# Kernel tuning notes

Hardware: AMD Instinct MI355X
Metric: run time of the kernel (lower is better)

## Reference

```python
import jax, jax.numpy as jnp
import numpy as np

N_NODES = 100000
N_EDGES = 1_600_000


def _glorot(key, shape):
    fan_in, fan_out = shape
    s = jnp.sqrt(6.0 / (fan_in + fan_out)).astype(jnp.float32)
    return jax.random.uniform(key, shape, jnp.float32, -1.0, 1.0) * s


def setup_inputs() -> dict:
    key = jax.random.key(0)
    ks = jax.random.split(key, 6)
    x = jax.random.normal(ks[0], (N_NODES, 88), jnp.float32)
    edge_index = jax.random.randint(ks[1], (2, N_EDGES), 0, N_NODES, dtype=jnp.int32)
    return {
        "x": x,
        "W1": _glorot(ks[2], (88, 65)), "b1": jnp.zeros((65,), jnp.float32),
        "W2": _glorot(ks[3], (65, 50)), "b2": jnp.zeros((50,), jnp.float32),
        "W3": _glorot(ks[4], (50, 65)), "b3": jnp.zeros((65,), jnp.float32),
        "W4": _glorot(ks[5], (65, 88)), "b4": jnp.zeros((88,), jnp.float32),
        "edge_index": edge_index,
    }


def _gcn_conv(h, W, b, src, dst, norm, n):
    # PyG GCNConv: transform, then normalized neighbor aggregation (self-loops
    # already folded into src/dst/norm).
    h = h @ W                                  # [N, out]
    msg = h[src] * norm[:, None]               # [E+N, out] gather
    return jax.ops.segment_sum(msg, dst, num_segments=n) + b  # scatter-add


def reference(x, W1, b1, W2, b2, W3, b3, W4, b4, edge_index):
    n = x.shape[0]
    loop = jnp.arange(n, dtype=edge_index.dtype)
    src = jnp.concatenate([edge_index[0], loop])   # add self-loops
    dst = jnp.concatenate([edge_index[1], loop])
    deg = jax.ops.segment_sum(jnp.ones_like(dst, dtype=x.dtype), dst, num_segments=n)
    dinv = jnp.where(deg > 0, jax.lax.rsqrt(deg), 0.0)
    norm = dinv[src] * dinv[dst]                   # D^-1/2 (A+I) D^-1/2 edge weights

    # encoder
    h = jax.nn.relu(_gcn_conv(x, W1, b1, src, dst, norm, n))
    h = _gcn_conv(h, W2, b2, src, dst, norm, n)
    # decoder
    h = jax.nn.relu(_gcn_conv(h, W3, b3, src, dst, norm, n))
    return _gcn_conv(h, W4, b4, src, dst, norm, n)
```

## Files before the change

kernel.cpp:

```cpp
#include <hip/hip_runtime.h>

#define BS 256
#define FB 1024
#define NB 256
#define CHUNK 4096
#define CAP 64
#define LCAP 8192

using half4 = __attribute__((ext_vector_type(4))) _Float16;

template<typename T>
__device__ __forceinline__ float4 load4(const T* p) {
    if constexpr (sizeof(T) == 4) {
        return *(const float4*)p;
    } else {
        half4 v = *(const half4*)p;
        return make_float4((float)v.x, (float)v.y, (float)v.z, (float)v.w);
    }
}
template<typename T>
__device__ __forceinline__ void store4(T* p, float4 v) {
    if constexpr (sizeof(T) == 4) {
        *(float4*)p = v;
    } else {
        half4 h = {(_Float16)v.x, (_Float16)v.y, (_Float16)v.z, (_Float16)v.w};
        *(half4*)p = h;
    }
}


__global__ __launch_bounds__(BS) void k_zero1(int* a, int n) {
    int i = blockIdx.x * BS + threadIdx.x;
    if (i < n) a[i] = 0;
}

__global__ __launch_bounds__(BS) void k_bucket(const int* __restrict__ src, const int* __restrict__ dst,
                                               unsigned* __restrict__ bbuf, int* __restrict__ bcounts,
                                               int E, unsigned long long invB, int bsz) {
    __shared__ int lcnt[NB];
    for (int t = threadIdx.x; t < NB; t += BS) lcnt[t] = 0;
    __syncthreads();
    int base_e = blockIdx.x * CHUNK;
    unsigned* mybuf = bbuf + (size_t)blockIdx.x * NB * CAP;
    #pragma unroll
    for (int j = 0; j < CHUNK / BS; ++j) {
        int e = base_e + j * BS + threadIdx.x;
        if (e < E) {
            int d = dst[e];
            int s = src[e];
            int b = (int)(((unsigned long long)(unsigned)d * invB) >> 40);
            int doff = d - b * bsz;
            int pos = atomicAdd(&lcnt[b], 1);
            if (pos < CAP)
                mybuf[b * CAP + pos] = ((unsigned)doff << 17) | (unsigned)s;
        }
    }
    __syncthreads();
    for (int t = threadIdx.x; t < NB; t += BS)
        bcounts[blockIdx.x * NB + t] = min(lcnt[t], CAP);
}

__global__ __launch_bounds__(FB) void k_cnt(const unsigned* __restrict__ bbuf, const int* __restrict__ bcounts,
                                            int* __restrict__ cnt, int nch, int bsz, int N) {
    __shared__ int lhist[512];
    for (int t = threadIdx.x; t < 512; t += FB) lhist[t] = 0;
    __syncthreads();
    int b = blockIdx.x;
    int lo = b * bsz;
    int total = nch * CAP;
    for (int idx = threadIdx.x; idx < total; idx += FB) {
        int seg = idx >> 6, slot = idx & 63;
        int c = bcounts[seg * NB + b];
        if (slot < c)
            atomicAdd(&lhist[bbuf[((size_t)seg * NB + b) * CAP + slot] >> 17], 1);
    }
    __syncthreads();
    int hi = min(N, lo + bsz);
    for (int t = threadIdx.x; t < hi - lo; t += FB) cnt[lo + t] = lhist[t];
}

__global__ __launch_bounds__(BS) void k_dinv(const int* __restrict__ cnt, float* __restrict__ dinv, int N) {
    int i = blockIdx.x * BS + threadIdx.x;
    if (i < N) dinv[i] = rsqrtf((float)(cnt[i] + 1));
}

__global__ __launch_bounds__(BS) void k_scan1(const int* __restrict__ cnt, int* __restrict__ bsum, int N) {
    __shared__ int s[BS];
    int i = blockIdx.x * BS + threadIdx.x;
    s[threadIdx.x] = (i < N) ? cnt[i] : 0;
    __syncthreads();
    for (int off = BS / 2; off > 0; off >>= 1) {
        if (threadIdx.x < off) s[threadIdx.x] += s[threadIdx.x + off];
        __syncthreads();
    }
    if (threadIdx.x == 0) bsum[blockIdx.x] = s[0];
}

__global__ __launch_bounds__(512) void k_scan2(int* bsum, int nb) {
    __shared__ int s[512];
    int t = threadIdx.x;
    int v = (t < nb) ? bsum[t] : 0;
    s[t] = v;
    __syncthreads();
    for (int off = 1; off < 512; off <<= 1) {
        int u = (t >= off) ? s[t - off] : 0;
        __syncthreads();
        s[t] += u;
        __syncthreads();
    }
    if (t < nb) bsum[t] = s[t] - v;
}

__global__ __launch_bounds__(BS) void k_scan3(const int* __restrict__ cnt, const int* __restrict__ boff,
                                              int* __restrict__ row_ptr, int N) {
    __shared__ int s[BS];
    int t = threadIdx.x;
    int i = blockIdx.x * BS + t;
    int v = (i < N) ? cnt[i] : 0;
    s[t] = v;
    __syncthreads();
    for (int off = 1; off < BS; off <<= 1) {
        int u = (t >= off) ? s[t - off] : 0;
        __syncthreads();
        s[t] += u;
        __syncthreads();
    }
    int base = boff[blockIdx.x];
    if (i < N) row_ptr[i] = base + s[t] - v;
    if (i == N - 1) row_ptr[N] = base + s[t];
}

__global__ __launch_bounds__(FB) void k_fill2(const unsigned* __restrict__ bbuf, const int* __restrict__ bcounts,
                                              const int* __restrict__ row_ptr, const float* __restrict__ dinv,
                                              uint2* __restrict__ entries,
                                              int nch, int bsz, int N) {
    __shared__ int cur[512];
    __shared__ float ldinv[512];
    __shared__ unsigned sorted[LCAP];

    int b = blockIdx.x;
    int lo = b * bsz;
    int hi = min(N, lo + bsz);
    int gbase = row_ptr[lo];
    int tot = row_ptr[hi] - gbase;
    for (int t = threadIdx.x; t < hi - lo; t += FB) {
        cur[t] = row_ptr[lo + t] - gbase;
        ldinv[t] = dinv[lo + t];
    }
    __syncthreads();

    int total = nch * CAP;
    for (int idx = threadIdx.x; idx < total; idx += FB) {
        int seg = idx >> 6, slot = idx & 63;
        int c = bcounts[seg * NB + b];
        if (slot < c) {
            unsigned u = bbuf[((size_t)seg * NB + b) * CAP + slot];
            int p = atomicAdd(&cur[u >> 17], 1);
            if (p < LCAP) sorted[p] = u;
        }
    }
    __syncthreads();

    for (int t = threadIdx.x; t < tot; t += FB) {
        unsigned u = sorted[t];
        int s = (int)(u & 0x1FFFFu);
        int doff = (int)(u >> 17);
        float w = dinv[s] * ldinv[doff];
        entries[gbase + t] = make_uint2((unsigned)s, __float_as_uint(w));
    }
}

template<typename TIN, int K, int M, int LDIN, int LDOUT, bool BIAS, bool RELU, typename TOUT>
__global__ __launch_bounds__(BS) void k_gemm(const TIN* __restrict__ H, const float* __restrict__ Wg,
                                             const float* __restrict__ bias, TOUT* __restrict__ out, int N) {
    constexpr int M4 = (M + 3) & ~3;
    __shared__ float Wl[K * M4];
    for (int idx = threadIdx.x; idx < K * M4; idx += BS) {
        int k = idx / M4, m = idx - k * M4;
        Wl[idx] = (m < M) ? Wg[(size_t)k * M + m] : 0.f;
    }
    __syncthreads();

    int row = blockIdx.x * BS + threadIdx.x;
    bool ok = row < N;
    int rr = ok ? row : (N - 1);
    const TIN* hp = H + (size_t)rr * LDIN;

    float acc[M4];
    #pragma unroll
    for (int m = 0; m < M4; ++m) acc[m] = 0.f;

    constexpr int K4 = K & ~3;
    #pragma unroll 2
    for (int k = 0; k < K4; k += 4) {
        float4 hv = load4(hp + k);
        const float h[4] = {hv.x, hv.y, hv.z, hv.w};
        #pragma unroll
        for (int j = 0; j < 4; ++j) {
            const float* wl = &Wl[(k + j) * M4];
            #pragma unroll
            for (int m = 0; m < M4; m += 4) {
                float4 w = *(const float4*)(wl + m);
                acc[m + 0] = fmaf(h[j], w.x, acc[m + 0]);
                acc[m + 1] = fmaf(h[j], w.y, acc[m + 1]);
                acc[m + 2] = fmaf(h[j], w.z, acc[m + 2]);
                acc[m + 3] = fmaf(h[j], w.w, acc[m + 3]);
            }
        }
    }
    #pragma unroll
    for (int k = K4; k < K; ++k) {
        float h = (float)hp[k];
        const float* wl = &Wl[k * M4];
        #pragma unroll
        for (int m = 0; m < M4; m += 4) {
            float4 w = *(const float4*)(wl + m);
            acc[m + 0] = fmaf(h, w.x, acc[m + 0]);
            acc[m + 1] = fmaf(h, w.y, acc[m + 1]);
            acc[m + 2] = fmaf(h, w.z, acc[m + 2]);
            acc[m + 3] = fmaf(h, w.w, acc[m + 3]);
        }
    }

    if (!ok) return;
    TOUT* op = out + (size_t)row * LDOUT;
    #pragma unroll
    for (int g = 0; g < LDOUT / 4; ++g) {
        int cb = 4 * g;
        float4 v;
        float* vp = &v.x;
        #pragma unroll
        for (int j = 0; j < 4; ++j) {
            int c = cb + j;
            float x = (c < M) ? acc[(c < M4) ? c : 0] : 0.f;
            if (BIAS && c < M) x += bias[c];
            if (RELU) x = fmaxf(x, 0.f);
            vp[j] = x;
        }
        store4(op + cb, v);
    }
}

template<typename TIN, typename TOUT, int M, int M4, int LDI, int LDO, bool BIAS, bool RELU>
__global__ __launch_bounds__(BS) void k_agg(const TIN* __restrict__ T, TOUT* __restrict__ out,
                                            const int* __restrict__ row_ptr, const uint2* __restrict__ entries,
                                            const float* __restrict__ dinv, const float* __restrict__ bias,
                                            int N) {
    constexpr int CG = M4 / 4;
    int idx = blockIdx.x * BS + threadIdx.x;
    if (idx >= N * CG) return;
    int i  = idx / CG;
    int cg = idx - i * CG;
    int c0 = cg * 4;

    float di = dinv[i];
    float4 t0 = load4(T + (size_t)i * LDI + c0);
    float w0 = di * di;
    float4 acc0 = make_float4(w0 * t0.x, w0 * t0.y, w0 * t0.z, w0 * t0.w);
    float4 acc1 = make_float4(0.f, 0.f, 0.f, 0.f);

    int e0 = row_ptr[i], e1 = row_ptr[i + 1];
    int e = e0;
    for (; e + 3 < e1; e += 4) {
        uint2 ea = entries[e];
        uint2 eb = entries[e + 1];
        uint2 ec = entries[e + 2];
        uint2 ed = entries[e + 3];
        float4 ta = load4(T + (size_t)ea.x * LDI + c0);
        float4 tb = load4(T + (size_t)eb.x * LDI + c0);
        float4 tc = load4(T + (size_t)ec.x * LDI + c0);
        float4 td = load4(T + (size_t)ed.x * LDI + c0);
        float wa = __uint_as_float(ea.y), wb = __uint_as_float(eb.y);
        float wc = __uint_as_float(ec.y), wd = __uint_as_float(ed.y);
        acc0.x = fmaf(wa, ta.x, acc0.x); acc0.y = fmaf(wa, ta.y, acc0.y);
        acc0.z = fmaf(wa, ta.z, acc0.z); acc0.w = fmaf(wa, ta.w, acc0.w);
        acc1.x = fmaf(wb, tb.x, acc1.x); acc1.y = fmaf(wb, tb.y, acc1.y);
        acc1.z = fmaf(wb, tb.z, acc1.z); acc1.w = fmaf(wb, tb.w, acc1.w);
        acc0.x = fmaf(wc, tc.x, acc0.x); acc0.y = fmaf(wc, tc.y, acc0.y);
        acc0.z = fmaf(wc, tc.z, acc0.z); acc0.w = fmaf(wc, tc.w, acc0.w);
        acc1.x = fmaf(wd, td.x, acc1.x); acc1.y = fmaf(wd, td.y, acc1.y);
        acc1.z = fmaf(wd, td.z, acc1.z); acc1.w = fmaf(wd, td.w, acc1.w);
    }
    for (; e < e1; ++e) {
        uint2 ea = entries[e];
        float4 ta = load4(T + (size_t)ea.x * LDI + c0);
        float wa = __uint_as_float(ea.y);
        acc0.x = fmaf(wa, ta.x, acc0.x); acc0.y = fmaf(wa, ta.y, acc0.y);
        acc0.z = fmaf(wa, ta.z, acc0.z); acc0.w = fmaf(wa, ta.w, acc0.w);
    }
    acc0.x += acc1.x; acc0.y += acc1.y; acc0.z += acc1.z; acc0.w += acc1.w;

    float* vp = &acc0.x;
    #pragma unroll
    for (int j = 0; j < 4; ++j) {
        if (BIAS && (c0 + j) < M) vp[j] += bias[c0 + j];
        if (RELU) vp[j] = fmaxf(vp[j], 0.f);
    }
    store4(out + (size_t)i * LDO + c0, acc0);
}


extern "C" void kernel_launch(void* const* d_in, const int* in_sizes, int n_in,
                              void* d_out, int out_size, void* d_ws, size_t ws_size,
                              hipStream_t stream) {
    const float* x  = (const float*)d_in[0];
    const float* W1 = (const float*)d_in[1];
    const float* b1 = (const float*)d_in[2];
    const float* W2 = (const float*)d_in[3];
    const float* b2 = (const float*)d_in[4];
    const float* W3 = (const float*)d_in[5];
    const float* b3 = (const float*)d_in[6];
    const float* W4 = (const float*)d_in[7];
    const float* b4 = (const float*)d_in[8];
    const int* edge_index = (const int*)d_in[9];

    const int N = in_sizes[0] / 88;
    const int E = in_sizes[9] / 2;
    const int* src = edge_index;
    const int* dst = edge_index + E;

    const int nch = (E + CHUNK - 1) / CHUNK;
    const int bsz = (N + NB - 1) / NB;
    const unsigned long long invB = ((1ull << 40) + bsz - 1) / bsz;

    char* p = (char*)d_ws;
    auto carve = [&](size_t bytes) { void* r = p; p += (bytes + 255) & ~(size_t)255; return r; };
    int*   cnt     = (int*)  carve((size_t)N * 4);
    float* dinv    = (float*)carve((size_t)N * 4);
    int*   row_ptr = (int*)  carve((size_t)(N + 1) * 4);
    int*   bsum    = (int*)  carve(4096);
    int*   bcounts = (int*)  carve((size_t)nch * NB * 4);
    unsigned* bbuf = (unsigned*)carve((size_t)nch * NB * CAP * 4);
    uint2* entries = (uint2*)carve((size_t)E * 8);
    _Float16* hA   = (_Float16*)carve((size_t)N * 68 * 2);
    _Float16* hB   = (_Float16*)carve((size_t)N * 68 * 2);
    _Float16* hC   = (_Float16*)carve((size_t)N * 68 * 2);

    int gN = (N + BS - 1) / BS;

    k_zero1 <<<gN, BS, 0, stream>>>(cnt, N);
    k_bucket<<<nch, BS, 0, stream>>>(src, dst, bbuf, bcounts, E, invB, bsz);
    k_cnt   <<<NB, FB, 0, stream>>>(bbuf, bcounts, cnt, nch, bsz, N);
    k_dinv  <<<gN, BS, 0, stream>>>(cnt, dinv, N);
    k_scan1 <<<gN, BS, 0, stream>>>(cnt, bsum, N);
    k_scan2 <<<1, 512, 0, stream>>>(bsum, gN);
    k_scan3 <<<gN, BS, 0, stream>>>(cnt, bsum, row_ptr, N);
    k_fill2 <<<NB, FB, 0, stream>>>(bbuf, bcounts, row_ptr, dinv, entries, nch, bsz, N);

    auto agg_grid = [&](int CG) { return (N * CG + BS - 1) / BS; };

    k_gemm<float, 88, 65, 88, 68, false, false, _Float16><<<gN, BS, 0, stream>>>(x, W1, nullptr, hA, N);
    k_agg<_Float16, _Float16, 65, 68, 68, 68, true, true><<<agg_grid(17), BS, 0, stream>>>(hA, hB, row_ptr, entries, dinv, b1, N);
    k_gemm<_Float16, 65, 50, 68, 64, false, false, _Float16><<<gN, BS, 0, stream>>>(hB, W2, nullptr, hC, N);
    k_agg<_Float16, _Float16, 50, 52, 64, 64, true, false><<<agg_grid(13), BS, 0, stream>>>(hC, hA, row_ptr, entries, dinv, b2, N);
    k_agg<_Float16, _Float16, 50, 52, 64, 52, false, false><<<agg_grid(13), BS, 0, stream>>>(hA, hB, row_ptr, entries, dinv, nullptr, N);
    k_gemm<_Float16, 50, 65, 52, 68, true, true, _Float16><<<gN, BS, 0, stream>>>(hB, W3, b3, hC, N);
    k_agg<_Float16, _Float16, 65, 68, 68, 68, false, false><<<agg_grid(17), BS, 0, stream>>>(hC, hA, row_ptr, entries, dinv, nullptr, N);
    k_gemm<_Float16, 65, 88, 68, 88, true, false, float><<<gN, BS, 0, stream>>>(hA, W4, b4, (float*)d_out, N);
}
```

Before: 491.7 us.

## Split dense GEMM work so each thread computes two rows by four columns

The node-feature GEMM used to give each thread one full output row, holding every output column in registers. It now gives each thread a 4-column group for two adjacent rows, and the launch grid is sized to match. This spreads the work over many more threads and cuts per-thread register pressure, which should raise occupancy and improve load-balancing. In exchange, each input row is loaded redundantly by several threads (mostly served from cache), and padding columns beyond M4 are no longer zero-filled.

Result: slower. 810.3 us (+64.8%).

```diff
diff --git a/kernel.cpp b/kernel.cpp
--- a/kernel.cpp
+++ b/kernel.cpp
@@ -170,10 +170,16 @@
     }
 }
 
+__device__ __forceinline__ void fma4(float4& a, float s, float4 w) {
+    a.x = fmaf(s, w.x, a.x); a.y = fmaf(s, w.y, a.y);
+    a.z = fmaf(s, w.z, a.z); a.w = fmaf(s, w.w, a.w);
+}
+
 template<typename TIN, int K, int M, int LDIN, int LDOUT, bool BIAS, bool RELU, typename TOUT>
 __global__ __launch_bounds__(BS) void k_gemm(const TIN* __restrict__ H, const float* __restrict__ Wg,
                                              const float* __restrict__ bias, TOUT* __restrict__ out, int N) {
     constexpr int M4 = (M + 3) & ~3;
+    constexpr int CG = M4 / 4;
     __shared__ float Wl[K * M4];
     for (int idx = threadIdx.x; idx < K * M4; idx += BS) {
         int k = idx / M4, m = idx - k * M4;
@@ -181,64 +187,58 @@
     }
     __syncthreads();
 
-    int row = blockIdx.x * BS + threadIdx.x;
-    bool ok = row < N;
-    int rr = ok ? row : (N - 1);
-    const TIN* hp = H + (size_t)rr * LDIN;
-
-    float acc[M4];
-    #pragma unroll
-    for (int m = 0; m < M4; ++m) acc[m] = 0.f;
+    int nrb = (N + 1) >> 1;
+    int idx = blockIdx.x * BS + threadIdx.x;
+    if (idx >= nrb * CG) return;
+    int rb = idx / CG;
+    int cg = idx - rb * CG;
+    int c0 = cg * 4;
+    int r0 = rb * 2;
+    bool two = (r0 + 1 < N);
+    int r1 = two ? r0 + 1 : r0;
+    const TIN* h0 = H + (size_t)r0 * LDIN;
+    const TIN* h1 = H + (size_t)r1 * LDIN;
+
+    float4 a0 = make_float4(0.f, 0.f, 0.f, 0.f);
+    float4 a1 = make_float4(0.f, 0.f, 0.f, 0.f);
 
     constexpr int K4 = K & ~3;
-    #pragma unroll 2
+    #pragma unroll
     for (int k = 0; k < K4; k += 4) {
-        float4 hv = load4(hp + k);
-        const float h[4] = {hv.x, hv.y, hv.z, hv.w};
-        #pragma unroll
-        for (int j = 0; j < 4; ++j) {
-            const float* wl = &Wl[(k + j) * M4];
-            #pragma unroll
-            for (int m = 0; m < M4; m += 4) {
-                float4 w = *(const float4*)(wl + m);
-                acc[m + 0] = fmaf(h[j], w.x, acc[m + 0]);
-                acc[m + 1] = fmaf(h[j], w.y, acc[m + 1]);
-                acc[m + 2] = fmaf(h[j], w.z, acc[m + 2]);
-                acc[m + 3] = fmaf(h[j], w.w, acc[m + 3]);
-            }
-        }
+        float4 p = load4(h0 + k);
+        float4 q = load4(h1 + k);
+        const float* wl = &Wl[k * M4 + c0];
+        float4 w0 = *(const float4*)(wl);
+        float4 w1 = *(const float4*)(wl + M4);
+        float4 w2 = *(const float4*)(wl + 2 * M4);
+        float4 w3 = *(const float4*)(wl + 3 * M4);
+        fma4(a0, p.x, w0); fma4(a1, q.x, w0);
+        fma4(a0, p.y, w1); fma4(a1, q.y, w1);
+        fma4(a0, p.z, w2); fma4(a1, q.z, w2);
+        fma4(a0, p.w, w3); fma4(a1, q.w, w3);
     }
     #pragma unroll
     for (int k = K4; k < K; ++k) {
-        float h = (float)hp[k];
-        const float* wl = &Wl[k * M4];
-        #pragma unroll
-        for (int m = 0; m < M4; m += 4) {
-            float4 w = *(const float4*)(wl + m);
-            acc[m + 0] = fmaf(h, w.x, acc[m + 0]);
-            acc[m + 1] = fmaf(h, w.y, acc[m + 1]);
-            acc[m + 2] = fmaf(h, w.z, acc[m + 2]);
-            acc[m + 3] = fmaf(h, w.w, acc[m + 3]);
-        }
-    }
-
-    if (!ok) return;
-    TOUT* op = out + (size_t)row * LDOUT;
-    #pragma unroll
-    for (int g = 0; g < LDOUT / 4; ++g) {
-        int cb = 4 * g;
-        float4 v;
-        float* vp = &v.x;
-        #pragma unroll
-        for (int j = 0; j < 4; ++j) {
-            int c = cb + j;
-            float x = (c < M) ? acc[(c < M4) ? c : 0] : 0.f;
-            if (BIAS && c < M) x += bias[c];
-            if (RELU) x = fmaxf(x, 0.f);
-            vp[j] = x;
-        }
-        store4(op + cb, v);
-    }
+        float p = (float)h0[k];
+        float q = (float)h1[k];
+        float4 w = *(const float4*)&Wl[k * M4 + c0];
+        fma4(a0, p, w); fma4(a1, q, w);
+    }
+
+    float* p0 = &a0.x;
+    float* p1 = &a1.x;
+    #pragma unroll
+    for (int j = 0; j < 4; ++j) {
+        int c = c0 + j;
+        bool in = (c < M);
+        float bb = (BIAS && in) ? bias[c] : 0.f;
+        float v0 = in ? p0[j] + bb : 0.f;
+        float v1 = in ? p1[j] + bb : 0.f;
+        if (RELU) { v0 = fmaxf(v0, 0.f); v1 = fmaxf(v1, 0.f); }
+        p0[j] = v0; p1[j] = v1;
+    }
+    store4(out + (size_t)r0 * LDOUT + c0, a0);
+    if (two) store4(out + (size_t)r1 * LDOUT + c0, a1);
 }
 
 template<typename TIN, typename TOUT, int M, int M4, int LDI, int LDO, bool BIAS, bool RELU>
@@ -347,14 +347,16 @@
     k_scan3 <<<gN, BS, 0, stream>>>(cnt, bsum, row_ptr, N);
     k_fill2 <<<NB, FB, 0, stream>>>(bbuf, bcounts, row_ptr, dinv, entries, nch, bsz, N);
 
-    auto agg_grid = [&](int CG) { return (N * CG + BS - 1) / BS; };
-
-    k_gemm<float, 88, 65, 88, 68, false, false, _Float16><<<gN, BS, 0, stream>>>(x, W1, nullptr, hA, N);
+    auto agg_grid  = [&](int CG) { return (N * CG + BS - 1) / BS; };
+    auto gemm_grid = [&](int M)  { int M4 = (M + 3) & ~3; int CG = M4 / 4;
+                                   return (((N + 1) / 2) * CG + BS - 1) / BS; };
+
+    k_gemm<float, 88, 65, 88, 68, false, false, _Float16><<<gemm_grid(65), BS, 0, stream>>>(x, W1, nullptr, hA, N);
     k_agg<_Float16, _Float16, 65, 68, 68, 68, true, true><<<agg_grid(17), BS, 0, stream>>>(hA, hB, row_ptr, entries, dinv, b1, N);
-    k_gemm<_Float16, 65, 50, 68, 64, false, false, _Float16><<<gN, BS, 0, stream>>>(hB, W2, nullptr, hC, N);
+    k_gemm<_Float16, 65, 50, 68, 64, false, false, _Float16><<<gemm_grid(50), BS, 0, stream>>>(hB, W2, nullptr, hC, N);
     k_agg<_Float16, _Float16, 50, 52, 64, 64, true, false><<<agg_grid(13), BS, 0, stream>>>(hC, hA, row_ptr, entries, dinv, b2, N);
     k_agg<_Float16, _Float16, 50, 52, 64, 52, false, false><<<agg_grid(13), BS, 0, stream>>>(hA, hB, row_ptr, entries, dinv, nullptr, N);
-    k_gemm<_Float16, 50, 65, 52, 68, true, true, _Float16><<<gN, BS, 0, stream>>>(hB, W3, b3, hC, N);
+    k_gemm<_Float16, 50, 65, 52, 68, true, true, _Float16><<<gemm_grid(65), BS, 0, stream>>>(hB, W3, b3, hC, N);
     k_agg<_Float16, _Float16, 65, 68, 68, 68, false, false><<<agg_grid(17), BS, 0, stream>>>(hC, hA, row_ptr, entries, dinv, nullptr, N);
-    k_gemm<_Float16, 65, 88, 68, 88, true, false, float><<<gN, BS, 0, stream>>>(hA, W4, b4, (float*)d_out, N);
-}
+    k_gemm<_Float16, 65, 88, 68, 88, true, false, float><<<gemm_grid(88), BS, 0, stream>>>(hA, W4, b4, (float*)d_out, N);
+}
```
